# Performance work log

Measured on AMD Instinct MI355X. Metric: run time of the kernel, lower is better.

The kernel has to match this reference:

```python
import jax, jax.numpy as jnp
import numpy as np

EPS = 1e-5
SIGMA = 1.0

def _conv(x, w, stride):
    return jax.lax.conv_general_dilated(
        x, w, window_strides=(stride, stride),
        padding=[(w.shape[2] // 2, w.shape[2] // 2), (w.shape[3] // 2, w.shape[3] // 2)],
        dimension_numbers=('NCHW', 'OIHW', 'NCHW'))

def _bn(x, gamma, beta, mean, var):
    # inference-mode batchnorm over channel dim (NCHW)
    inv = gamma / jnp.sqrt(var + EPS)
    return x * inv[None, :, None, None] + (beta - mean * inv)[None, :, None, None]

def setup_inputs() -> dict:
    key = jax.random.key(0)
    ks = jax.random.split(key, 8)
    B, M, H, W, K = 8, 128, 64, 64, 6
    x = jax.random.normal(ks[0], (B, M, H, W), jnp.float32)
    cf = jax.random.normal(ks[1], (B, M, H, W), jnp.float32)
    w1 = jax.random.normal(ks[2], (M // 2, M, 3, 3), jnp.float32) * 0.05
    w2 = jax.random.normal(ks[3], (M // 4, M // 2, 3, 3), jnp.float32) * 0.05
    w3 = jax.random.normal(ks[4], (K, M // 4, 1, 1), jnp.float32) * 0.05
    def bn_params(k, c):
        k1, k2 = jax.random.split(k)
        return (jnp.ones((c,), jnp.float32),
                jnp.zeros((c,), jnp.float32),
                jax.random.normal(k1, (c,), jnp.float32) * 0.1,
                jnp.abs(jax.random.normal(k2, (c,), jnp.float32)) * 0.1 + 1.0)
    g1, b1, m1, v1 = bn_params(ks[5], M // 2)
    g2, b2, m2, v2 = bn_params(ks[6], M // 4)
    g3, b3, m3, v3 = bn_params(ks[7], K)
    return dict(x=x, center_features=cf, w1=w1, g1=g1, b1=b1, m1=m1, v1=v1,
                w2=w2, g2=g2, b2=b2, m2=m2, v2=v2,
                w3=w3, g3=g3, b3=b3, m3=m3, v3=v3)

def reference(x, center_features, w1, g1, b1, m1, v1, w2, g2, b2, m2, v2, w3, g3, b3, m3, v3):
    # center branch: conv-bn-relu x2 (stride 2) + 1x1 conv-bn, then spatial mean
    c = jax.nn.relu(_bn(_conv(center_features, w1, 2), g1, b1, m1, v1))
    c = jax.nn.relu(_bn(_conv(c, w2, 2), g2, b2, m2, v2))
    c = _bn(_conv(c, w3, 1), g3, b3, m3, v3)
    centers = c.reshape(c.shape[0], c.shape[1], -1).mean(axis=2)  # [B, K]

    B, C, H, W = x.shape
    K = centers.shape[-1]
    xf = x.reshape(B, C, H * W, 1)                      # [B,C,HW,1]
    cb = centers[:, None, None, :]                      # [B,1,1,K]
    dist = (xf - cb) ** 2                               # [B,C,HW,K]
    phi_soft = jax.nn.softmax(-SIGMA * dist, axis=-1)
    qsoft = jnp.sum(phi_soft * cb, axis=-1).reshape(B, C, H, W)
    symbols = jnp.argmin(dist, axis=-1)                 # [B,C,HW] (== argmax of hard softmax)
    qhard = centers[jnp.arange(B)[:, None, None], symbols].reshape(B, C, H, W)
    qbar = qsoft + jax.lax.stop_gradient(qhard - qsoft)
    return qbar, qsoft, qhard, symbols.reshape(B, C, H, W), centers
```

## Files before the change

kernel.cpp:

```cpp
#include <hip/hip_runtime.h>
#include <math.h>

#define BN_EPS 1e-5
#define SIGMA 1.0f

__global__ __launch_bounds__(256, 4) void conv1_partial_kernel(
    const float* __restrict__ in, const float* __restrict__ w1,
    float* __restrict__ part)
{
    __shared__ double wlds[1152];

    int bid = blockIdx.x;
    int oht = bid & 1;
    int b   = (bid >> 1) & 7;
    int isp = (bid >> 4) & 7;
    int ocg = bid >> 7;

    int tid = threadIdx.x;
    int ow  = tid & 31;
    int ohp = tid >> 5;
    int oh0 = oht * 16 + ohp * 2;
    int ih0 = 2 * oh0 - 1;
    int iw0 = 2 * ow - 1;

    for (int i = tid; i < 1152; i += 256) {
        int j  = i & 7;
        int t  = i >> 3;
        int k  = t % 9;
        int ic = t / 9;
        wlds[i] = (double)w1[((ocg * 8 + j) * 128 + isp * 16 + ic) * 9 + k];
    }
    __syncthreads();

    double acc0[8], acc1[8];
    #pragma unroll
    for (int j = 0; j < 8; ++j) { acc0[j] = 0.0; acc1[j] = 0.0; }

    bool rowok[5], colok[3];
    #pragma unroll
    for (int t = 0; t < 5; ++t) rowok[t] = (ih0 + t) >= 0;
    #pragma unroll
    for (int t = 0; t < 3; ++t) colok[t] = (iw0 + t) >= 0;

    const float* base0 = in + ((size_t)(b * 128 + isp * 16) * 64 + ih0) * 64 + iw0;

    float cur[15];
    #pragma unroll
    for (int t = 0; t < 5; ++t)
        #pragma unroll
        for (int kw = 0; kw < 3; ++kw)
            cur[t * 3 + kw] = (rowok[t] && colok[kw]) ? base0[t * 64 + kw] : 0.f;

    for (int ic = 0; ic < 16; ++ic) {
        float nxt[15];
        if (ic + 1 < 16) {
            const float* basen = base0 + (size_t)(ic + 1) * 4096;
            #pragma unroll
            for (int t = 0; t < 5; ++t)
                #pragma unroll
                for (int kw = 0; kw < 3; ++kw)
                    nxt[t * 3 + kw] = (rowok[t] && colok[kw]) ? basen[t * 64 + kw] : 0.f;
        }
        double xv[15];
        #pragma unroll
        for (int i = 0; i < 15; ++i) xv[i] = (double)cur[i];

        const double* wk = &wlds[ic * 72];
        #pragma unroll
        for (int k = 0; k < 9; ++k) {
            int kh = k / 3, kw = k % 3;
            double2 wa = *(const double2*)&wk[k * 8 + 0];
            double2 wb = *(const double2*)&wk[k * 8 + 2];
            double2 wc = *(const double2*)&wk[k * 8 + 4];
            double2 wd = *(const double2*)&wk[k * 8 + 6];
            double x0 = xv[kh * 3 + kw];
            double x1 = xv[(kh + 2) * 3 + kw];
            acc0[0] = fma(x0, wa.x, acc0[0]);  acc1[0] = fma(x1, wa.x, acc1[0]);
            acc0[1] = fma(x0, wa.y, acc0[1]);  acc1[1] = fma(x1, wa.y, acc1[1]);
            acc0[2] = fma(x0, wb.x, acc0[2]);  acc1[2] = fma(x1, wb.x, acc1[2]);
            acc0[3] = fma(x0, wb.y, acc0[3]);  acc1[3] = fma(x1, wb.y, acc1[3]);
            acc0[4] = fma(x0, wc.x, acc0[4]);  acc1[4] = fma(x1, wc.x, acc1[4]);
            acc0[5] = fma(x0, wc.y, acc0[5]);  acc1[5] = fma(x1, wc.y, acc1[5]);
            acc0[6] = fma(x0, wd.x, acc0[6]);  acc1[6] = fma(x1, wd.x, acc1[6]);
            acc0[7] = fma(x0, wd.y, acc0[7]);  acc1[7] = fma(x1, wd.y, acc1[7]);
        }
        #pragma unroll
        for (int i = 0; i < 15; ++i) cur[i] = nxt[i];
    }

    #pragma unroll
    for (int j = 0; j < 8; ++j) {
        int idx0 = ((b * 64 + ocg * 8 + j) * 32 + oh0) * 32 + ow;
        part[isp * 524288 + idx0]      = (float)acc0[j];
        part[isp * 524288 + idx0 + 32] = (float)acc1[j];
    }
}

__global__ __launch_bounds__(256) void conv1_combine_kernel(
    const float* __restrict__ part,
    const float* __restrict__ g, const float* __restrict__ be,
    const float* __restrict__ mn, const float* __restrict__ vr,
    float* __restrict__ y1)
{
    int idx = blockIdx.x * 256 + threadIdx.x;
    int oc = (idx >> 10) & 63;
    double s = 0.0;
    #pragma unroll
    for (int p = 0; p < 8; ++p) s += (double)part[idx + p * 524288];
    double inv = (double)g[oc] / sqrt((double)vr[oc] + BN_EPS);
    double o = s * inv + ((double)be[oc] - (double)mn[oc] * inv);
    y1[idx] = fmaxf((float)o, 0.f);
}

__global__ __launch_bounds__(256) void conv2_partial_kernel(
    const float* __restrict__ y1, const float* __restrict__ w,
    float* __restrict__ part)
{
    __shared__ float tin[4][33][36];
    __shared__ float twt[4][9][8];

    int bid = blockIdx.x;
    int ocg = bid & 3;
    int b   = (bid >> 2) & 7;
    int isp = bid >> 5;

    int tid = threadIdx.x;
    int ow  = tid & 15;
    int oh  = tid >> 4;

    const float* inb = y1 + (size_t)(b * 64 + isp * 4) * 1024;

    for (int lin = tid; lin < 4 * 33 * 34; lin += 256) {
        int c   = lin % 34;
        int t2  = lin / 34;
        int rr  = t2 % 33;
        int icc = t2 / 33;
        int ih  = rr - 1;
        int iw  = c - 1;
        float v = 0.f;
        if ((unsigned)ih < 32u && (unsigned)iw < 32u)
            v = inb[(icc * 32 + ih) * 32 + iw];
        tin[icc][rr][c] = v;
    }
    for (int i = tid; i < 288; i += 256) {
        int j   = i & 7;
        int k   = (i >> 3) % 9;
        int icc = i / 72;
        twt[icc][k][j] = w[(ocg * 8 + j) * 576 + (isp * 4 + icc) * 9 + k];
    }
    __syncthreads();

    double acc[8];
    #pragma unroll
    for (int j = 0; j < 8; ++j) acc[j] = 0.0;

    for (int icc = 0; icc < 4; ++icc) {
        double xv[9];
        #pragma unroll
        for (int kh = 0; kh < 3; ++kh)
            #pragma unroll
            for (int kw = 0; kw < 3; ++kw)
                xv[kh * 3 + kw] = (double)tin[icc][2 * oh + kh][2 * ow + kw];
        #pragma unroll
        for (int k = 0; k < 9; ++k) {
            float4 wa = *(const float4*)&twt[icc][k][0];
            float4 wb = *(const float4*)&twt[icc][k][4];
            acc[0] = fma(xv[k], (double)wa.x, acc[0]);
            acc[1] = fma(xv[k], (double)wa.y, acc[1]);
            acc[2] = fma(xv[k], (double)wa.z, acc[2]);
            acc[3] = fma(xv[k], (double)wa.w, acc[3]);
            acc[4] = fma(xv[k], (double)wb.x, acc[4]);
            acc[5] = fma(xv[k], (double)wb.y, acc[5]);
            acc[6] = fma(xv[k], (double)wb.z, acc[6]);
            acc[7] = fma(xv[k], (double)wb.w, acc[7]);
        }
    }
    int obase = ((b * 32 + ocg * 8) * 16 + oh) * 16 + ow;
    #pragma unroll
    for (int j = 0; j < 8; ++j)
        part[isp * 65536 + obase + j * 256] = (float)acc[j];
}

__global__ __launch_bounds__(256) void conv2_combine_ybar_kernel(
    const float* __restrict__ part,
    const float* __restrict__ g, const float* __restrict__ be,
    const float* __restrict__ mn, const float* __restrict__ vr,
    double* __restrict__ ybar)
{
    __shared__ double sm[4];
    int j  = blockIdx.x;
    int oc = j & 31;
    int t  = threadIdx.x;
    int idx = j * 256 + t;
    double s = 0.0;
    #pragma unroll
    for (int p = 0; p < 16; ++p) s += (double)part[idx + p * 65536];
    double inv = (double)g[oc] / sqrt((double)vr[oc] + BN_EPS);
    double o = s * inv + ((double)be[oc] - (double)mn[oc] * inv);
    double v = fmax(o, 0.0);
    #pragma unroll
    for (int off = 32; off > 0; off >>= 1) v += __shfl_down(v, off, 64);
    if ((t & 63) == 0) sm[t >> 6] = v;
    __syncthreads();
    if (t == 0) ybar[j] = (sm[0] + sm[1] + sm[2] + sm[3]) * (1.0 / 256.0);
}

__global__ __launch_bounds__(64) void centers_kernel(
    const double* __restrict__ ybar, const float* __restrict__ w3,
    const float* __restrict__ g, const float* __restrict__ be,
    const float* __restrict__ mn, const float* __restrict__ vr,
    double* __restrict__ cen_ws, float* __restrict__ cen_out)
{
    int t = threadIdx.x;
    if (t < 48) {
        int b = t / 6;
        int k = t % 6;
        double acc = 0.0;
        for (int ic = 0; ic < 32; ++ic) acc = fma((double)w3[k * 32 + ic], ybar[b * 32 + ic], acc);
        double inv = (double)g[k] / sqrt((double)vr[k] + BN_EPS);
        double c = acc * inv + ((double)be[k] - (double)mn[k] * inv);
        cen_ws[t]  = c;
        cen_out[t] = (float)c;
    }
}

__global__ __launch_bounds__(256) void quant_kernel(
    const float* __restrict__ x, const double* __restrict__ centers,
    float* __restrict__ qbar, float* __restrict__ qsoft,
    float* __restrict__ qhard, float* __restrict__ sym)
{
    int vid = blockIdx.x * 256 + threadIdx.x;
    int b = vid >> 17;

    double c[6];
    float cf[6];
    #pragma unroll
    for (int k = 0; k < 6; ++k) { c[k] = centers[b * 6 + k]; cf[k] = (float)c[k]; }

    float4 xv = ((const float4*)x)[vid];
    float xs[4] = {xv.x, xv.y, xv.z, xv.w};
    float r_bar[4], r_soft[4], r_hard[4], r_sym[4];

    #pragma unroll
    for (int i = 0; i < 4; ++i) {
        double xx = (double)xs[i];
        double d[6];
        double dmin = 1e300;
        int amin = 0;
        #pragma unroll
        for (int k = 0; k < 6; ++k) {
            double t = xx - c[k];
            d[k] = t * t;
            if (d[k] < dmin) { dmin = d[k]; amin = k; }
        }
        float se = 0.f, sw = 0.f;
        #pragma unroll
        for (int k = 0; k < 6; ++k) {
            float e = __expf(SIGMA * (float)(dmin - d[k]));
            se += e;
            sw += e * cf[k];
        }
        float qs = sw / se;
        float qh = cf[amin];
        r_soft[i] = qs;
        r_hard[i] = qh;
        r_bar[i]  = qh;
        r_sym[i]  = (float)amin;
    }

    ((float4*)qbar)[vid]  = make_float4(r_bar[0],  r_bar[1],  r_bar[2],  r_bar[3]);
    ((float4*)qsoft)[vid] = make_float4(r_soft[0], r_soft[1], r_soft[2], r_soft[3]);
    ((float4*)qhard)[vid] = make_float4(r_hard[0], r_hard[1], r_hard[2], r_hard[3]);
    ((float4*)sym)[vid]   = make_float4(r_sym[0],  r_sym[1],  r_sym[2],  r_sym[3]);
}

extern "C" void kernel_launch(void* const* d_in, const int* in_sizes, int n_in,
                              void* d_out, int out_size, void* d_ws, size_t ws_size,
                              hipStream_t stream) {
    const float* x  = (const float*)d_in[0];
    const float* cf = (const float*)d_in[1];
    const float* w1 = (const float*)d_in[2];
    const float* g1 = (const float*)d_in[3];
    const float* b1 = (const float*)d_in[4];
    const float* m1 = (const float*)d_in[5];
    const float* v1 = (const float*)d_in[6];
    const float* w2 = (const float*)d_in[7];
    const float* g2 = (const float*)d_in[8];
    const float* b2 = (const float*)d_in[9];
    const float* m2 = (const float*)d_in[10];
    const float* v2 = (const float*)d_in[11];
    const float* w3 = (const float*)d_in[12];
    const float* g3 = (const float*)d_in[13];
    const float* b3 = (const float*)d_in[14];
    const float* m3 = (const float*)d_in[15];
    const float* v3 = (const float*)d_in[16];

    const int NELEM = 8 * 128 * 64 * 64;
    float* out   = (float*)d_out;
    float* qbar  = out;
    float* qsoft = out + (size_t)NELEM;
    float* qhard = out + (size_t)2 * NELEM;
    float* sym   = out + (size_t)3 * NELEM;
    float* cen_o = out + (size_t)4 * NELEM;

    char* ws = (char*)d_ws;
    float*  part1 = (float*)(ws);
    float*  y1    = (float*)(ws + 16777216);
    float*  part2 = (float*)(ws + 18874368);
    double* yb    = (double*)(ws + 23068672);
    double* cen   = (double*)(ws + 23070720);

    conv1_partial_kernel<<<1024, 256, 0, stream>>>(cf, w1, part1);
    conv1_combine_kernel<<<2048, 256, 0, stream>>>(part1, g1, b1, m1, v1, y1);
    conv2_partial_kernel<<<512, 256, 0, stream>>>(y1, w2, part2);
    conv2_combine_ybar_kernel<<<256, 256, 0, stream>>>(part2, g2, b2, m2, v2, yb);
    centers_kernel<<<1, 64, 0, stream>>>(yb, w3, g3, b3, m3, v3, cen, cen_o);
    quant_kernel<<<NELEM / 4 / 256, 256, 0, stream>>>(x, cen, qbar, qsoft, qhard, sym);
}
```

Before: 180.7 us.

## Split conv1 input channels 16 ways and fuse centers into quant kernel

Conv1 partial kernel now splits the 128 input channels into 16 slices of 8 instead of 8 slices of 16. This doubles the grid to 2048 blocks, halves the LDS weight tile and raises the occupancy hint, trading more partial-sum traffic in the combine kernel (16 reads per output) for more parallelism. The separate single-block centers kernel is removed. Every quant block now recomputes the 48 centers from ybar into shared memory, which drops one launch but repeats a small amount of work per block.

Result: slower. 240.3 us (+33.0%).

```diff
diff --git a/kernel.cpp b/kernel.cpp
--- a/kernel.cpp
+++ b/kernel.cpp
@@ -4,17 +4,17 @@
 #define BN_EPS 1e-5
 #define SIGMA 1.0f
 
-__global__ __launch_bounds__(256, 4) void conv1_partial_kernel(
+__global__ __launch_bounds__(256, 8) void conv1_partial_kernel(
     const float* __restrict__ in, const float* __restrict__ w1,
     float* __restrict__ part)
 {
-    __shared__ double wlds[1152];
+    __shared__ double wlds[576];
 
     int bid = blockIdx.x;
     int oht = bid & 1;
     int b   = (bid >> 1) & 7;
-    int isp = (bid >> 4) & 7;
-    int ocg = bid >> 7;
+    int isp = (bid >> 4) & 15;
+    int ocg = bid >> 8;
 
     int tid = threadIdx.x;
     int ow  = tid & 31;
@@ -23,12 +23,12 @@
     int ih0 = 2 * oh0 - 1;
     int iw0 = 2 * ow - 1;
 
-    for (int i = tid; i < 1152; i += 256) {
+    for (int i = tid; i < 576; i += 256) {
         int j  = i & 7;
         int t  = i >> 3;
         int k  = t % 9;
         int ic = t / 9;
-        wlds[i] = (double)w1[((ocg * 8 + j) * 128 + isp * 16 + ic) * 9 + k];
+        wlds[i] = (double)w1[((ocg * 8 + j) * 128 + isp * 8 + ic) * 9 + k];
     }
     __syncthreads();
 
@@ -42,7 +42,7 @@
     #pragma unroll
     for (int t = 0; t < 3; ++t) colok[t] = (iw0 + t) >= 0;
 
-    const float* base0 = in + ((size_t)(b * 128 + isp * 16) * 64 + ih0) * 64 + iw0;
+    const float* base0 = in + ((size_t)(b * 128 + isp * 8) * 64 + ih0) * 64 + iw0;
 
     float cur[15];
     #pragma unroll
@@ -51,9 +51,9 @@
         for (int kw = 0; kw < 3; ++kw)
             cur[t * 3 + kw] = (rowok[t] && colok[kw]) ? base0[t * 64 + kw] : 0.f;
 
-    for (int ic = 0; ic < 16; ++ic) {
+    for (int ic = 0; ic < 8; ++ic) {
         float nxt[15];
-        if (ic + 1 < 16) {
+        if (ic + 1 < 8) {
             const float* basen = base0 + (size_t)(ic + 1) * 4096;
             #pragma unroll
             for (int t = 0; t < 5; ++t)
@@ -106,7 +106,7 @@
     int oc = (idx >> 10) & 63;
     double s = 0.0;
     #pragma unroll
-    for (int p = 0; p < 8; ++p) s += (double)part[idx + p * 524288];
+    for (int p = 0; p < 16; ++p) s += (double)part[idx + p * 524288];
     double inv = (double)g[oc] / sqrt((double)vr[oc] + BN_EPS);
     double o = s * inv + ((double)be[oc] - (double)mn[oc] * inv);
     y1[idx] = fmaxf((float)o, 0.f);
@@ -205,37 +205,37 @@
     if (t == 0) ybar[j] = (sm[0] + sm[1] + sm[2] + sm[3]) * (1.0 / 256.0);
 }
 
-__global__ __launch_bounds__(64) void centers_kernel(
-    const double* __restrict__ ybar, const float* __restrict__ w3,
+__global__ __launch_bounds__(256) void quant_kernel(
+    const float* __restrict__ x, const double* __restrict__ ybar,
+    const float* __restrict__ w3,
     const float* __restrict__ g, const float* __restrict__ be,
     const float* __restrict__ mn, const float* __restrict__ vr,
-    double* __restrict__ cen_ws, float* __restrict__ cen_out)
-{
-    int t = threadIdx.x;
-    if (t < 48) {
-        int b = t / 6;
-        int k = t % 6;
+    float* __restrict__ qbar, float* __restrict__ qsoft,
+    float* __restrict__ qhard, float* __restrict__ sym,
+    float* __restrict__ cen_out)
+{
+    __shared__ double cen[48];
+    int tid = threadIdx.x;
+    if (tid < 48) {
+        int bb = tid / 6;
+        int k  = tid % 6;
         double acc = 0.0;
-        for (int ic = 0; ic < 32; ++ic) acc = fma((double)w3[k * 32 + ic], ybar[b * 32 + ic], acc);
+        for (int ic = 0; ic < 32; ++ic)
+            acc = fma((double)w3[k * 32 + ic], ybar[bb * 32 + ic], acc);
         double inv = (double)g[k] / sqrt((double)vr[k] + BN_EPS);
         double c = acc * inv + ((double)be[k] - (double)mn[k] * inv);
-        cen_ws[t]  = c;
-        cen_out[t] = (float)c;
-    }
-}
-
-__global__ __launch_bounds__(256) void quant_kernel(
-    const float* __restrict__ x, const double* __restrict__ centers,
-    float* __restrict__ qbar, float* __restrict__ qsoft,
-    float* __restrict__ qhard, float* __restrict__ sym)
-{
-    int vid = blockIdx.x * 256 + threadIdx.x;
+        cen[tid] = c;
+        if (blockIdx.x == 0) cen_out[tid] = (float)c;
+    }
+    __syncthreads();
+
+    int vid = blockIdx.x * 256 + tid;
     int b = vid >> 17;
 
     double c[6];
     float cf[6];
     #pragma unroll
-    for (int k = 0; k < 6; ++k) { c[k] = centers[b * 6 + k]; cf[k] = (float)c[k]; }
+    for (int k = 0; k < 6; ++k) { c[k] = cen[b * 6 + k]; cf[k] = (float)c[k]; }
 
     float4 xv = ((const float4*)x)[vid];
     float xs[4] = {xv.x, xv.y, xv.z, xv.w};
@@ -305,15 +305,14 @@
 
     char* ws = (char*)d_ws;
     float*  part1 = (float*)(ws);
-    float*  y1    = (float*)(ws + 16777216);
-    float*  part2 = (float*)(ws + 18874368);
-    double* yb    = (double*)(ws + 23068672);
-    double* cen   = (double*)(ws + 23070720);
-
-    conv1_partial_kernel<<<1024, 256, 0, stream>>>(cf, w1, part1);
+    float*  y1    = (float*)(ws + 33554432);
+    float*  part2 = (float*)(ws + 35651584);
+    double* yb    = (double*)(ws + 39845888);
+
+    conv1_partial_kernel<<<2048, 256, 0, stream>>>(cf, w1, part1);
     conv1_combine_kernel<<<2048, 256, 0, stream>>>(part1, g1, b1, m1, v1, y1);
     conv2_partial_kernel<<<512, 256, 0, stream>>>(y1, w2, part2);
     conv2_combine_ybar_kernel<<<256, 256, 0, stream>>>(part2, g2, b2, m2, v2, yb);
-    centers_kernel<<<1, 64, 0, stream>>>(yb, w3, g3, b3, m3, v3, cen, cen_o);
-    quant_kernel<<<NELEM / 4 / 256, 256, 0, stream>>>(x, cen, qbar, qsoft, qhard, sym);
-}
+    quant_kernel<<<NELEM / 4 / 256, 256, 0, stream>>>(x, yb, w3, g3, b3, m3, v3,
+                                                      qbar, qsoft, qhard, sym, cen_o);
+}
```
